# Kernel optimization log

Measured on AMD Instinct MI355X. Metric: run time of the kernel, lower is better.

Reference implementation:

```python
import jax, jax.numpy as jnp
import numpy as np

# BiDiGemma (Aveygo/SRNext) wrapping RecurrentGemma-style ResidualBlocks:
#   block0 = RECURRENT (causal conv width 4 + RG-LRU linear recurrence)
#   block1 = local (sliding-window, MQA) ATTENTION with partial RoPE
# Dropout(0.1) is treated as eval-mode identity.

B, S, D, H = 4, 4096, 256, 4
HD = D // H            # head dim = 64
E = 3 * D              # mlp_expanded_width = expand_ratio * dim
W_ATT = D              # attention_window_size = dim = 256 (divides S)
TW = 4                 # recurrentgemma temporal conv width
_NEG = -2.3819763e38   # recurrentgemma masking constant

_PNAMES = ["ln_gamma","ln_beta","proj_w","proj_b","fconv_w","fconv_b","bconv_w","bconv_b",
 "rn0_t","rn0_c","ly_w","ly_b","lx_w","lx_b","lo_w","lo_b","c1d_w","c1d_b",
 "a_param","ig_w","ig_b","ag_w","ag_b","mlp0_up_w","mlp0_up_b","mlp0_dn_w","mlp0_dn_b",
 "rn1_t","rn1_c","q_w","k_w","v_w","o_w","o_b","mlp1_up_w","mlp1_up_b","mlp1_dn_w","mlp1_dn_b"]


def _init_params(key):
    ks = iter(jax.random.split(key, 24))
    nrm = lambda shape, s: jax.random.normal(next(ks), shape, jnp.float32) * s
    p = {}
    p["ln_gamma"] = jnp.ones((D,), jnp.float32); p["ln_beta"] = jnp.zeros((D,), jnp.float32)
    p["proj_w"] = nrm((D, D), D ** -0.5);  p["proj_b"] = jnp.zeros((D,), jnp.float32)
    p["fconv_w"] = nrm((D, D), D ** -0.5); p["fconv_b"] = jnp.zeros((D,), jnp.float32)
    p["bconv_w"] = nrm((D, D), D ** -0.5); p["bconv_b"] = jnp.zeros((D,), jnp.float32)
    p["rn0_t"] = jnp.zeros((D,), jnp.float32); p["rn0_c"] = jnp.zeros((D,), jnp.float32)
    p["ly_w"] = nrm((D, D), D ** -0.5); p["ly_b"] = jnp.zeros((D,), jnp.float32)
    p["lx_w"] = nrm((D, D), D ** -0.5); p["lx_b"] = jnp.zeros((D,), jnp.float32)
    p["lo_w"] = nrm((D, D), D ** -0.5); p["lo_b"] = jnp.zeros((D,), jnp.float32)
    p["c1d_w"] = nrm((TW, D), 0.1);     p["c1d_b"] = jnp.zeros((D,), jnp.float32)
    p["a_param"] = jnp.log(jnp.expm1(jnp.linspace(0.9, 1.5, D, dtype=jnp.float32)))
    p["ig_w"] = nrm((H, HD, HD), HD ** -0.5); p["ig_b"] = jnp.zeros((H, HD), jnp.float32)
    p["ag_w"] = nrm((H, HD, HD), HD ** -0.5); p["ag_b"] = jnp.zeros((H, HD), jnp.float32)
    p["mlp0_up_w"] = nrm((2, D, E), D ** -0.5); p["mlp0_up_b"] = jnp.zeros((2, E), jnp.float32)
    p["mlp0_dn_w"] = nrm((E, D), E ** -0.5);    p["mlp0_dn_b"] = jnp.zeros((D,), jnp.float32)
    p["rn1_t"] = jnp.zeros((D,), jnp.float32); p["rn1_c"] = jnp.zeros((D,), jnp.float32)
    p["q_w"] = nrm((D, D), D ** -0.5); p["k_w"] = nrm((D, HD), D ** -0.5); p["v_w"] = nrm((D, HD), D ** -0.5)
    p["o_w"] = nrm((D, D), D ** -0.5); p["o_b"] = jnp.zeros((D,), jnp.float32)
    p["mlp1_up_w"] = nrm((2, D, E), D ** -0.5); p["mlp1_up_b"] = jnp.zeros((2, E), jnp.float32)
    p["mlp1_dn_w"] = nrm((E, D), E ** -0.5);    p["mlp1_dn_b"] = jnp.zeros((D,), jnp.float32)
    return p


def _gelu(x):
    return jax.nn.gelu(x, approximate=False)  # torch F.gelu default (erf)


def _rms_norm(x, scale, eps=1e-6):
    var = jnp.mean(jnp.square(x), axis=-1, keepdims=True)
    return x * jax.lax.rsqrt(var + eps) * (1.0 + scale)


def _layer_norm(x, g, b, eps=1e-5):
    m = jnp.mean(x, axis=-1, keepdims=True)
    v = jnp.mean(jnp.square(x - m), axis=-1, keepdims=True)
    return (x - m) * jax.lax.rsqrt(v + eps) * g + b


def _block_diag(x, w, b):
    # BlockDiagonalLinear: per-head [HD x HD] blocks
    xh = x.reshape(*x.shape[:-1], H, HD)
    y = jnp.einsum('bshd,hdk->bshk', xh, w) + b
    return y.reshape(*x.shape)


def _causal_conv1d(x, w, b):
    # depthwise causal conv, w: [TW, D], w[TW-1] multiplies current token
    xp = jnp.pad(x, ((0, 0), (TW - 1, 0), (0, 0)))
    out = sum(xp[:, i:i + x.shape[1], :] * w[i] for i in range(TW))
    return out + b


def _rg_lru(x, pos, a_param, ig_w, ig_b, ag_w, ag_b):
    gate_x = jax.nn.sigmoid(_block_diag(x, ig_w, ig_b))
    gate_a = jax.nn.sigmoid(_block_diag(x, ag_w, ag_b))
    log_a = -8.0 * gate_a * jax.nn.softplus(a_param)   # c = 8
    a = jnp.exp(log_a)
    mult = jnp.sqrt(-jnp.expm1(2.0 * log_a))           # sqrt(1 - a^2)
    reset = (pos == 0)[..., None]
    mult = jnp.where(reset, 1.0, mult)
    bterm = x * gate_x * mult
    def comb(e1, e2):
        a1, b1 = e1
        a2, b2 = e2
        return a1 * a2, a2 * b1 + b2
    _, h = jax.lax.associative_scan(comb, (a, bterm), axis=1)
    return h


def _rope(x, pos):
    # partial RoPE: applied to first half of head dim (recurrentgemma)
    rot, rest = jnp.split(x, 2, axis=-1)
    f = rot.shape[-1] // 2
    inv_freq = 10000.0 ** (-(2.0 / rot.shape[-1]) * jnp.arange(f, dtype=jnp.float32))
    t = pos[..., None, None].astype(jnp.float32) * inv_freq  # [b, s, 1, f]
    sin, cos = jnp.sin(t), jnp.cos(t)
    x1, x2 = jnp.split(rot, 2, axis=-1)
    return jnp.concatenate([x1 * cos - x2 * sin, x2 * cos + x1 * sin, rest], axis=-1)


def _local_attention(x, pos, q_w, k_w, v_w, o_w, o_b):
    # MQA sliding-window attention, window = W_ATT; chunked to honor locality
    b, s, _ = x.shape
    q = (x @ q_w).reshape(b, s, H, HD)
    k = (x @ k_w).reshape(b, s, 1, HD)
    v = (x @ v_w).reshape(b, s, HD)
    q = _rope(q, pos) * (HD ** -0.5)
    k = _rope(k, pos)[:, :, 0]
    Wn = W_ATT
    nb = s // Wn
    qc = q.reshape(b, nb, Wn, H, HD)
    kp = jnp.pad(k, ((0, 0), (Wn, 0), (0, 0))).reshape(b, nb + 1, Wn, HD)
    vp = jnp.pad(v, ((0, 0), (Wn, 0), (0, 0))).reshape(b, nb + 1, Wn, HD)
    kc = jnp.concatenate([kp[:, :-1], kp[:, 1:]], axis=2)  # [b, nb, 2W, HD]
    vc = jnp.concatenate([vp[:, :-1], vp[:, 1:]], axis=2)
    logits = jnp.einsum('bnqhd,bnkd->bnhqk', qc, kc)
    i = jnp.arange(Wn)[:, None]
    j = jnp.arange(2 * Wn)[None, :]
    diff = (i + Wn) - j                       # q_pos - k_pos
    base = (diff >= 0) & (diff <= Wn)         # causal & q <= k + window_size
    cidx = jnp.arange(nb)[:, None, None]
    mask = base[None] & ((cidx > 0) | (j[None] >= Wn))  # no left padding in chunk 0
    logits = jnp.where(mask[None, :, None], logits, _NEG)
    probs = jax.nn.softmax(logits, axis=-1)
    out = jnp.einsum('bnhqk,bnkd->bnqhd', probs, vc).reshape(b, s, D)
    return out @ o_w + o_b


def _mlp(x, up_w, up_b, dn_w, dn_b):
    up = jnp.einsum('bsd,cde->cbse', x, up_w) + up_b[:, None, None, :]
    act = _gelu(up[0]) * up[1]
    return act @ dn_w + dn_b


def _gemma_block(x, pos, p):
    # ResidualBlock 0: RECURRENT
    raw = x
    xn = _rms_norm(raw, p['rn0_t'])
    y = _gelu(xn @ p['ly_w'] + p['ly_b'])
    xr = xn @ p['lx_w'] + p['lx_b']
    xr = _causal_conv1d(xr, p['c1d_w'], p['c1d_b'])
    xr = _rg_lru(xr, pos, p['a_param'], p['ig_w'], p['ig_b'], p['ag_w'], p['ag_b'])
    xr = (xr * y) @ p['lo_w'] + p['lo_b']
    residual = xr + raw
    x = _rms_norm(residual, p['rn0_c'])
    x = _mlp(x, p['mlp0_up_w'], p['mlp0_up_b'], p['mlp0_dn_w'], p['mlp0_dn_b']) + residual
    # ResidualBlock 1: local ATTENTION
    raw = x
    xn = _rms_norm(raw, p['rn1_t'])
    xa = _local_attention(xn, pos, p['q_w'], p['k_w'], p['v_w'], p['o_w'], p['o_b'])
    residual = xa + raw
    x = _rms_norm(residual, p['rn1_c'])
    x = _mlp(x, p['mlp1_up_w'], p['mlp1_up_b'], p['mlp1_dn_w'], p['mlp1_dn_b']) + residual
    return x


def _forward(skip, *params):
    p = dict(zip(_PNAMES, params))
    b, s, _ = skip.shape
    pos = jnp.broadcast_to(jnp.arange(s, dtype=jnp.int32)[None], (b, s))
    x = _layer_norm(skip, p['ln_gamma'], p['ln_beta']) @ p['proj_w'] + p['proj_b']
    z = jax.nn.sigmoid(jnp.mean(jax.nn.silu(skip), axis=-1, keepdims=True))
    fwd = _gemma_block(x @ p['fconv_w'] + p['fconv_b'], pos, p)  # Conv1d k=1 == pointwise
    bwd = _gemma_block(x @ p['bconv_w'] + p['bconv_b'], pos, p)
    return z * (fwd + bwd) + skip


def setup_inputs() -> dict:
    key = jax.random.key(0)
    kx, kp = jax.random.split(key)
    inp = {"skip": jax.random.normal(kx, (B, S, D), jnp.float32)}
    inp.update(_init_params(kp))
    return inp


def reference(skip, ln_gamma, ln_beta, proj_w, proj_b, fconv_w, fconv_b, bconv_w, bconv_b, rn0_t, rn0_c, ly_w, ly_b, lx_w, lx_b, lo_w, lo_b, c1d_w, c1d_b, a_param, ig_w, ig_b, ag_w, ag_b, mlp0_up_w, mlp0_up_b, mlp0_dn_w, mlp0_dn_b, rn1_t, rn1_c, q_w, k_w, v_w, o_w, o_b, mlp1_up_w, mlp1_up_b, mlp1_dn_w, mlp1_dn_b):
    return _forward(skip, ln_gamma, ln_beta, proj_w, proj_b, fconv_w, fconv_b, bconv_w, bconv_b, rn0_t, rn0_c, ly_w, ly_b, lx_w, lx_b, lo_w, lo_b, c1d_w, c1d_b, a_param, ig_w, ig_b, ag_w, ag_b, mlp0_up_w, mlp0_up_b, mlp0_dn_w, mlp0_dn_b, rn1_t, rn1_c, q_w, k_w, v_w, o_w, o_b, mlp1_up_w, mlp1_up_b, mlp1_dn_w, mlp1_dn_b)
```

## Files before the change

kernel.cpp:

```cpp
#include <hip/hip_runtime.h>
#include <math.h>
#include <stddef.h>


#define BB   4
#define SS   4096
#define DD   256
#define HH   4
#define HDIM 64
#define EE   768
#define RR   (BB*SS)
#define RR2  (2*RR)
#define WNN  256
#define CH   64
#define NCH  (SS/CH)

typedef __attribute__((ext_vector_type(8))) short bfrag;
typedef __attribute__((ext_vector_type(4))) float f4acc;

__device__ __forceinline__ float geluf(float x){
  float u = 1.5957691216f*(x + 0.044715f*x*x*x);
  float e = __expf(u);
  float t = 1.f - 2.f/(e+1.f);
  return 0.5f*x*(1.f+t);
// ... 179 lines not shown
      if constexpr(TERMS>=2){
        *(float4*)&Bsl[d0] = *(const float4*)(pB0l0 + k0);
        *(float4*)&Bsl[d1] = *(const float4*)(pB0l1 + k0);
      }
    } else {
      *(float4*)&Bsh[d0] = *(const float4*)(pBa + k0);
      if constexpr(TERMS>=2) *(float4*)&Bsl[d0] = *(const float4*)(pBb + k0);
      if constexpr(DUAL){
        *(float4*)&B2h[d0] = *(const float4*)(pBc + k0);
        if constexpr(TERMS>=2) *(float4*)&B2l[d0] = *(const float4*)(pBd + k0);
      }
    }
    __syncthreads();

    bfrag ah[4], al[TERMS==3?4:1], b0hf[NT], b0lf[TERMS>=2?NT:1];
    bfrag b1hf[DUAL?NT:1], b1lf[(DUAL&&TERMS>=2)?NT:1];
#pragma unroll
    for(int mi=0;mi<4;mi++){
      int row = wm*64 + mi*16 + m16;
      ah[mi] = *(const bfrag*)&Ash[row*ST + q*8];
      if constexpr(TERMS==3) al[mi] = *(const bfrag*)&Asl[row*ST + q*8];
    }
#pragma unroll
    for(int ni=0;ni<NT;ni++){
      int n = wn*(BN/2) + ni*16 + m16;
      b0hf[ni] = *(const bfrag*)&Bsh[n*ST + q*8];
      if constexpr(TERMS>=2) b0lf[ni] = *(const bfrag*)&Bsl[n*ST + q*8];
      if constexpr(DUAL){
        b1hf[ni] = *(const bfrag*)&B2h[n*ST + q*8];
        if constexpr(TERMS>=2) b1lf[ni] = *(const bfrag*)&B2l[n*ST + q*8];
      }
    }
#pragma unroll
    for(int mi=0;mi<4;mi++)
#pragma unroll
      for(int ni=0;ni<NT;ni++){
        acc[mi][ni] = __builtin_amdgcn_mfma_f32_16x16x32_bf16(ah[mi], b0hf[ni], acc[mi][ni],0,0,0);
        if constexpr(TERMS>=2)
          acc[mi][ni] = __builtin_amdgcn_mfma_f32_16x16x32_bf16(ah[mi], b0lf[ni], acc[mi][ni],0,0,0);
        if constexpr(TERMS==3)
          acc[mi][ni] = __builtin_amdgcn_mfma_f32_16x16x32_bf16(al[mi], b0hf[ni], acc[mi][ni],0,0,0);
        if constexpr(DUAL){
          acc2[mi][ni] = __builtin_amdgcn_mfma_f32_16x16x32_bf16(ah[mi], b1hf[ni], acc2[mi][ni],0,0,0);
          if constexpr(TERMS>=2)
            acc2[mi][ni] = __builtin_amdgcn_mfma_f32_16x16x32_bf16(ah[mi], b1lf[ni], acc2[mi][ni],0,0,0);
          if constexpr(TERMS==3)
            acc2[mi][ni] = __builtin_amdgcn_mfma_f32_16x16x32_bf16(al[mi], b1hf[ni], acc2[mi][ni],0,0,0);
        }
      }
    __syncthreads();
  }

  if constexpr(OUT==0 || OUT==1 || OUT==5){
#pragma unroll
    for(int ni=0;ni<NT;ni++){
      const int col = bn + wn*(BN/2) + ni*16 + m16;
      float bv0 = (MODE&1) ? bias0[col] : 0.f;
      float bv1 = DUAL ? bias1[col] : 0.f;
#pragma unroll
      for(int mi=0;mi<4;mi++){
#pragma unroll
        for(int r=0;r<4;r++){
          const int row = bm + wm*64 + mi*16 + q*4 + r;
          float v = acc[mi][ni][r] + bv0;
          if constexpr(DUAL){
            float v2 = acc2[mi][ni][r] + bv1;
            v = geluf(v) * v2;
          } else if(MODE&2){
            v = geluf(v);
          }
          if(MODE&8) v += Res[(size_t)row*ldc + col];
          if constexpr(OUT==0){
            C[(size_t)row*ldc + col] = v;
          } else if constexpr(OUT==1){
            unsigned short hb = f2bf(v);
            Ch[(size_t)row*ldc + col] = hb;
            Cl[(size_t)row*ldc + col] = f2bf(v - bf2f(hb));
          } else {
            Ch[(size_t)row*ldc + col] = f2bf(v);
          }
        }
      }
    }
  } else if constexpr(OUT==2){
    const int hb = bn + wn*64;
    const float p = (float)m16;
    const float invf = __expf(-p * 0.575646273248511f);
#pragma unroll
    for(int mi=0;mi<4;mi++){
#pragma unroll
      for(int r=0;r<4;r++){
        const int row = bm + wm*64 + mi*16 + q*4 + r;
        const int s = row & (SS-1);
        float t = (float)s * invf;
        float sn, cs; __sincosf(t, &sn, &cs);
        float x1 = acc[mi][0][r], x2 = acc[mi][1][r];
        float v0 = (x1*cs - x2*sn)*0.125f;
        float v1 = (x2*cs + x1*sn)*0.125f;
        float v2 = acc[mi][2][r]*0.125f;
        float v3 = acc[mi][3][r]*0.125f;
        size_t base = (size_t)row*ldc + hb;
        unsigned short hh;
        hh=f2bf(v0); Ch[base+m16]=hh;    Cl[base+m16]   =f2bf(v0-bf2f(hh));
        hh=f2bf(v1); Ch[base+16+m16]=hh; Cl[base+16+m16]=f2bf(v1-bf2f(hh));
        hh=f2bf(v2); Ch[base+32+m16]=hh; Cl[base+32+m16]=f2bf(v2-bf2f(hh));
        hh=f2bf(v3); Ch[base+48+m16]=hh; Cl[base+48+m16]=f2bf(v3-bf2f(hh));
      }
    }
  } else if constexpr(OUT==3){
    const float p = (float)m16;
    const float invf = __expf(-p * 0.575646273248511f);
#pragma unroll
    for(int mi=0;mi<4;mi++){
#pragma unroll
      for(int r=0;r<4;r++){
        const int row = bm + wm*64 + mi*16 + q*4 + r;
        const int s = row & (SS-1);
        float v0, v1;
        if(wn==0){
          float t = (float)s * invf;
          float sn, cs; __sincosf(t, &sn, &cs);
          float x1 = acc[mi][0][r], x2 = acc[mi][1][r];
          v0 = x1*cs - x2*sn;
          v1 = x2*cs + x1*sn;
        } else {
          v0 = acc[mi][0][r]; v1 = acc[mi][1][r];
        }
        size_t base = (size_t)row*ldc + wn*32;
        unsigned short hh;
        hh=f2bf(v0); Ch[base+m16]=hh;    Cl[base+m16]   =f2bf(v0-bf2f(hh));
        hh=f2bf(v1); Ch[base+16+m16]=hh; Cl[base+16+m16]=f2bf(v1-bf2f(hh));
      }
    }
  } else if constexpr(OUT==4){
#pragma unroll
    for(int ni=0;ni<NT;ni++){
      const int col = wn*32 + ni*16 + m16;
#pragma unroll
      for(int mi=0;mi<4;mi++){
        const int rowb = bm + wm*64 + mi*16 + q*4;
        const int b = rowb >> 12, sl = rowb & (SS-1);
        ushort4 hv;
        hv.x = f2bf(acc[mi][ni][0]); hv.y = f2bf(acc[mi][ni][1]);
        hv.z = f2bf(acc[mi][ni][2]); hv.w = f2bf(acc[mi][ni][3]);
        *(ushort4*)(Ch + ((size_t)(b*64 + col))*SS + sl) = hv;
      }
    }
  } else if constexpr(OUT==7){
    const float p = (float)m16;
    const float invf = __expf(-p * 0.575646273248511f);
#pragma unroll
    for(int mi=0;mi<4;mi++){
#pragma unroll
      for(int r=0;r<4;r++){
        const int row = bm + wm*64 + mi*16 + q*4 + r;
        const int s = row & (SS-1);
        float v0, v1;
        if(wn==0){
          float t = (float)s * invf;
          float sn, cs; __sincosf(t, &sn, &cs);
          float x1 = acc[mi][0][r], x2 = acc[mi][1][r];
          v0 = x1*cs - x2*sn;
          v1 = x2*cs + x1*sn;
        } else {
          v0 = acc[mi][0][r]; v1 = acc[mi][1][r];
        }
        size_t base = (size_t)row*ldc + wn*32;
        unsigned short hh;
        hh=f2bf(v0); Ch[base+m16]=hh;    Cl[base+m16]   =f2bf(v0-bf2f(hh));
        hh=f2bf(v1); Ch[base+16+m16]=hh; Cl[base+16+m16]=f2bf(v1-bf2f(hh));
      }
    }
    if constexpr(DUAL){
      unsigned short* Cv = (unsigned short*)C;
#pragma unroll
      for(int ni=0;ni<NT;ni++){
        const int col = wn*32 + ni*16 + m16;
#pragma unroll
        for(int mi=0;mi<4;mi++){
          const int rowb = bm + wm*64 + mi*16 + q*4;
          const int b = rowb >> 12, sl = rowb & (SS-1);
          ushort4 hv;
          hv.x = f2bf(acc2[mi][ni][0]); hv.y = f2bf(acc2[mi][ni][1]);
          hv.z = f2bf(acc2[mi][ni][2]); hv.w = f2bf(acc2[mi][ni][3]);
          *(ushort4*)(Cv + ((size_t)(b*64 + col))*SS + sl) = hv;
        }
      }
    }
  }
}

__global__ __launch_bounds__(256) void gates_conv_k(
    const float* __restrict__ X,
    const float* __restrict__ cw, const float* __restrict__ cb,
    const unsigned short* __restrict__ igth, const unsigned short* __restrict__ igtl,
    const unsigned short* __restrict__ agth, const unsigned short* __restrict__ agtl,
    const float* __restrict__ igb, const float* __restrict__ agb,
    const float* __restrict__ ap,
    float* __restrict__ Aout, float* __restrict__ Bout)
{
  constexpr int ST = 72;
  __shared__ unsigned short Ash[128*ST];
  __shared__ unsigned short Asl[128*ST];

  const int h  = blockIdx.x;
  const int bm = blockIdx.y*128;
  const int tid = threadIdx.x;
  const int lane = tid & 63, wave = tid >> 6;
  const int wm = wave >> 1, wn = wave & 1;
  const int m16 = lane & 15, q = lane >> 4;

  {
    const int strip = tid >> 4;
    const int cg = (tid & 15)*4;
    const int col0 = h*HDIM + cg;
    const int r0 = bm + strip*8;
    float h0[4], h1[4], h2[4];
#pragma unroll
    for(int i=0;i<3;i++){
      int rr = r0 - 3 + i;
      int rc = rr < 0 ? 0 : rr;
      float4 hv = *(const float4*)(X + (size_t)rc*DD + col0);
      float* dst = (i==0)?h0:((i==1)?h1:h2);
      dst[0]=hv.x; dst[1]=hv.y; dst[2]=hv.z; dst[3]=hv.w;
    }
    float4 w0v = *(const float4*)(cw + 0*DD + col0);
    float4 w1v = *(const float4*)(cw + 1*DD + col0);
    float4 w2v = *(const float4*)(cw + 2*DD + col0);
    float4 w3v = *(const float4*)(cw + 3*DD + col0);
    float4 bbv = *(const float4*)(cb + col0);
    const float* w0 = (const float*)&w0v; const float* w1 = (const float*)&w1v;
    const float* w2 = (const float*)&w2v; const float* w3 = (const float*)&w3v;
    const float* bb = (const float*)&bbv;
    for(int rr=0; rr<8; rr++){
      const int r = r0 + rr;
      const int s = r & (SS-1);
      float4 cv = *(const float4*)(X + (size_t)r*DD + col0);
      float cur[4]; cur[0]=cv.x; cur[1]=cv.y; cur[2]=cv.z; cur[3]=cv.w;
      ushort4 hi, lo;
      unsigned short* hp = (unsigned short*)&hi;
      unsigned short* lp = (unsigned short*)&lo;
#pragma unroll
      for(int j=0;j<4;j++){
        float acc = bb[j] + w3[j]*cur[j];
        if(s>=1) acc += w2[j]*h2[j];
        if(s>=2) acc += w1[j]*h1[j];
        if(s>=3) acc += w0[j]*h0[j];
        unsigned short hb = f2bf(acc);
        hp[j] = hb; lp[j] = f2bf(acc - bf2f(hb));
      }
      const int dst = (strip*8+rr)*ST + cg;
      *(ushort4*)&Ash[dst] = hi;
      *(ushort4*)&Asl[dst] = lo;
#pragma unroll
      for(int j=0;j<4;j++){ h0[j]=h1[j]; h1[j]=h2[j]; h2[j]=cur[j]; }
    }
  }
  __syncthreads();

  f4acc accI[4][2], accA[4][2];
#pragma unroll
  for(int i=0;i<4;i++)
#pragma unroll
    for(int j=0;j<2;j++){ accI[i][j]=(f4acc)0.f; accA[i][j]=(f4acc)0.f; }

  const size_t wbase = (size_t)h*HDIM*HDIM;
#pragma unroll
  for(int ks=0;ks<2;ks++){
    bfrag ah[4], al[4];
#pragma unroll
    for(int mi=0;mi<4;mi++){
      const int row = wm*64 + mi*16 + m16;
      ah[mi] = *(const bfrag*)&Ash[row*ST + ks*32 + q*8];
      al[mi] = *(const bfrag*)&Asl[row*ST + ks*32 + q*8];
    }
#pragma unroll
    for(int ni=0;ni<2;ni++){
      const size_t bo = wbase + (size_t)(wn*32 + ni*16 + m16)*HDIM + ks*32 + q*8;
      bfrag bIh = *(const bfrag*)(igth + bo);
      bfrag bIl = *(const bfrag*)(igtl + bo);
      bfrag bAh = *(const bfrag*)(agth + bo);
      bfrag bAl = *(const bfrag*)(agtl + bo);
#pragma unroll
      for(int mi=0;mi<4;mi++){
        accI[mi][ni] = __builtin_amdgcn_mfma_f32_16x16x32_bf16(ah[mi], bIh, accI[mi][ni],0,0,0);
        accI[mi][ni] = __builtin_amdgcn_mfma_f32_16x16x32_bf16(ah[mi], bIl, accI[mi][ni],0,0,0);
        accI[mi][ni] = __builtin_amdgcn_mfma_f32_16x16x32_bf16(al[mi], bIh, accI[mi][ni],0,0,0);
        accA[mi][ni] = __builtin_amdgcn_mfma_f32_16x16x32_bf16(ah[mi], bAh, accA[mi][ni],0,0,0);
        accA[mi][ni] = __builtin_amdgcn_mfma_f32_16x16x32_bf16(ah[mi], bAl, accA[mi][ni],0,0,0);
        accA[mi][ni] = __builtin_amdgcn_mfma_f32_16x16x32_bf16(al[mi], bAh, accA[mi][ni],0,0,0);
      }
    }
  }

#pragma unroll
  for(int ni=0;ni<2;ni++){
    const int cl  = wn*32 + ni*16 + m16;
    const int col = h*HDIM + cl;
    const float bI = igb[col], bA = agb[col];
    const float apv = ap[col];
    const float sp = (apv > 20.f) ? apv : log1pf(expf(apv));
#pragma unroll
    for(int mi=0;mi<4;mi++){
#pragma unroll
      for(int r=0;r<4;r++){
        const int lrow = wm*64 + mi*16 + q*4 + r;
        const int row = bm + lrow;
        const int s = row & (SS-1);
        float gx = 1.f/(1.f + __expf(-(accI[mi][ni][r] + bI)));
        float ga = 1.f/(1.f + __expf(-(accA[mi][ni][r] + bA)));
        float la = -8.f * ga * sp;
        float a_ = __expf(la);
        float mult = (s==0) ? 1.f : sqrtf(fmaxf(1.f - __expf(2.f*la), 0.f));
        float x = bf2f(Ash[lrow*ST + cl]) + bf2f(Asl[lrow*ST + cl]);
        Aout[(size_t)row*DD + col] = a_;
        Bout[(size_t)row*DD + col] = x * gx * mult;
      }
    }
  }
}

__global__ __launch_bounds__(256) void scan1_k(const float* __restrict__ A,
    const float* __restrict__ Bv, float* __restrict__ csa, float* __restrict__ csb)
{
  int idx = blockIdx.x*256 + threadIdx.x;
  int d = idx & (DD-1);
  int c = (idx >> 8) & (NCH-1);
  int b = idx >> 14;
  size_t base = ((size_t)b*SS + (size_t)c*CH)*DD + d;
  float Aa = 1.f, Bb_ = 0.f;
  for(int t=0;t<CH;t++){
    float a  = A [base + (size_t)t*DD];
    float bb = Bv[base + (size_t)t*DD];
    Aa  = a*Aa;
    Bb_ = a*Bb_ + bb;
  }
  csa[idx] = Aa; csb[idx] = Bb_;
}

__global__ __launch_bounds__(256) void scan2_k(const float* __restrict__ csa,
    float* __restrict__ csb)
{
  int idx = blockIdx.x*256 + threadIdx.x;
  int d = idx & (DD-1);
  int b = idx >> 8;
  float h = 0.f;
  for(int c=0;c<NCH;c++){
    size_t i = ((size_t)b*NCH + c)*DD + d;
    float Aa = csa[i], Bb_ = csb[i];
    csb[i] = h;
    h = Aa*h + Bb_;
  }
}

__global__ __launch_bounds__(256) void scan3_k(const float* __restrict__ A,
    const float* __restrict__ Bv, const float* __restrict__ csb,
    const unsigned short* __restrict__ Yh,
    unsigned short* __restrict__ Hh)
{
  int idx = blockIdx.x*256 + threadIdx.x;
  int d = idx & (DD-1);
  int c = (idx >> 8) & (NCH-1);
  int b = idx >> 14;
  size_t base = ((size_t)b*SS + (size_t)c*CH)*DD + d;
  float h = csb[idx];
  for(int t=0;t<CH;t++){
    float a  = A [base + (size_t)t*DD];
    float bb = Bv[base + (size_t)t*DD];
    h = a*h + bb;
    float v = h * bf2f(Yh[base + (size_t)t*DD]);
    Hh[base + (size_t)t*DD] = f2bf(v);
  }
}

#define AST 72
__global__ __launch_bounds__(256) void attn_k(
    const unsigned short* __restrict__ Qh, const unsigned short* __restrict__ Ql,
    const unsigned short* __restrict__ Kh, const unsigned short* __restrict__ Kl,
    const unsigned short* __restrict__ Vt,
    unsigned short* __restrict__ Oh, unsigned short* __restrict__ Ol)
{
  __shared__ unsigned short Ksh[64*AST], Ksl[64*AST], Vsh[64*AST];
  __shared__ unsigned short Ps[4*16*AST];

  const int qt = blockIdx.x & 3, n = blockIdx.x >> 2;
  const int h = blockIdx.y, b = blockIdx.z;
  const int tid = threadIdx.x;
  const int lane = tid & 63, w = tid >> 6;
  const int m16 = lane & 15, q = lane >> 4;
  const int s0 = n*WNN + qt*64;

  const size_t qro = ((size_t)(b*SS + s0 + w*16 + m16))*DD + h*HDIM + q*8;
  bfrag qh0 = *(const bfrag*)(Qh + qro);
  bfrag qh1 = *(const bfrag*)(Qh + qro + 32);
  bfrag ql0 = *(const bfrag*)(Ql + qro);
  bfrag ql1 = *(const bfrag*)(Ql + qro + 32);

  float mrow[4], lrow[4];
  f4acc oacc[4];
#pragma unroll
  for(int i=0;i<4;i++){ mrow[i]=-3.0e38f; lrow[i]=0.f; oacc[i]=(f4acc)0.f; }

  const int ktlo = (n==0) ? 4 : qt;
  const int kthi = qt + 4;
  const int sr = tid >> 2, sc = tid & 3;

  for(int kt=ktlo; kt<=kthi; kt++){
    const int kbase = (n-1)*WNN + kt*64;
#pragma unroll
    for(int cc=0; cc<2; cc++){
      int g = sc + cc*4;
      *(float4*)&Ksh[sr*AST + g*8] =
        *(const float4*)(Kh + (size_t)(b*SS + kbase + sr)*HDIM + g*8);
      *(float4*)&Ksl[sr*AST + g*8] =
        *(const float4*)(Kl + (size_t)(b*SS + kbase + sr)*HDIM + g*8);
      *(float4*)&Vsh[sr*AST + g*8] =
        *(const float4*)(Vt + ((size_t)(b*64 + sr))*SS + kbase + g*8);
    }
    __syncthreads();

    f4acc sacc[4];
#pragma unroll
    for(int nt=0;nt<4;nt++) sacc[nt] = (f4acc)0.f;
#pragma unroll
    for(int nt=0;nt<4;nt++){
      const int kr = (nt*16+m16)*AST;
      bfrag kh0 = *(const bfrag*)&Ksh[kr + q*8];
      bfrag kh1 = *(const bfrag*)&Ksh[kr + 32 + q*8];
      bfrag kl0 = *(const bfrag*)&Ksl[kr + q*8];
      bfrag kl1 = *(const bfrag*)&Ksl[kr + 32 + q*8];
      sacc[nt] = __builtin_amdgcn_mfma_f32_16x16x32_bf16(qh0, kh0, sacc[nt],0,0,0);
      sacc[nt] = __builtin_amdgcn_mfma_f32_16x16x32_bf16(qh0, kl0, sacc[nt],0,0,0);
      sacc[nt] = __builtin_amdgcn_mfma_f32_16x16x32_bf16(ql0, kh0, sacc[nt],0,0,0);
      sacc[nt] = __builtin_amdgcn_mfma_f32_16x16x32_bf16(qh1, kh1, sacc[nt],0,0,0);
      sacc[nt] = __builtin_amdgcn_mfma_f32_16x16x32_bf16(qh1, kl1, sacc[nt],0,0,0);
      sacc[nt] = __builtin_amdgcn_mfma_f32_16x16x32_bf16(ql1, kh1, sacc[nt],0,0,0);
    }

    const bool needlo = (kt == qt+4);
    const bool needhi = (kt == qt);
#pragma unroll
    for(int r=0;r<4;r++){
      int qp = qt*64 + w*16 + q*4 + r;
      float sv[4];
      float tm = -3.0e38f;
#pragma unroll
      for(int nt=0;nt<4;nt++){
        float scv = sacc[nt][r];
        if(needlo || needhi){
          int kj = kt*64 + nt*16 + m16;
          int diff = qp + WNN - kj;
          bool ok = (!needlo || diff >= 0) && (!needhi || diff <= WNN);
          scv = ok ? scv : -3.0e38f;
        }
        sv[nt] = scv;
        tm = fmaxf(tm, scv);
      }
#pragma unroll
      for(int off=1; off<16; off<<=1) tm = fmaxf(tm, __shfl_xor(tm, off, 64));
      float mn = fmaxf(mrow[r], tm);
      float alpha = __expf(mrow[r]-mn);
      float rs = 0.f;
#pragma unroll
      for(int nt=0;nt<4;nt++){
        float pp = __expf(sv[nt]-mn);
        rs += pp;
        Ps[w*16*AST + (q*4+r)*AST + nt*16 + m16] = f2bf(pp);
      }
#pragma unroll
      for(int off=1; off<16; off<<=1) rs += __shfl_xor(rs, off, 64);
      lrow[r] = lrow[r]*alpha + rs;
      mrow[r] = mn;
#pragma unroll
      for(int nt=0;nt<4;nt++) oacc[nt][r] *= alpha;
    }

#pragma unroll
    for(int s=0;s<2;s++){
      bfrag pa = *(const bfrag*)&Ps[w*16*AST + m16*AST + s*32 + q*8];
#pragma unroll
      for(int nt=0;nt<4;nt++){
        bfrag vh_ = *(const bfrag*)&Vsh[(nt*16+m16)*AST + s*32 + q*8];
        oacc[nt] = __builtin_amdgcn_mfma_f32_16x16x32_bf16(pa, vh_, oacc[nt],0,0,0);
      }
    }
    __syncthreads();
  }

#pragma unroll
  for(int r=0;r<4;r++){
    float invl = 1.f/lrow[r];
    const size_t rowbase = ((size_t)(b*SS + s0 + w*16 + q*4 + r))*DD + h*HDIM;
#pragma unroll
    for(int nt=0;nt<4;nt++){
      float v = oacc[nt][r]*invl;
      unsigned short hb = f2bf(v);
      Oh[rowbase + nt*16 + m16] = hb;
      Ol[rowbase + nt*16 + m16] = f2bf(v - bf2f(hb));
    }
  }
}

__global__ __launch_bounds__(256) void comb_k(const float* __restrict__ of,
    const float* __restrict__ ob, const float* __restrict__ z,
    const float* __restrict__ skip, float* __restrict__ out)
{
  int idx = blockIdx.x*256 + threadIdx.x;
  int r = idx >> 8;
  out[idx] = z[r]*(of[idx]+ob[idx]) + skip[idx];
}

struct Params {
  const float *ln_gamma,*ln_beta,*proj_w,*proj_b,*fconv_w,*fconv_b,*bconv_w,*bconv_b,
    *rn0_t,*rn0_c,*ly_w,*ly_b,*lx_w,*lx_b,*lo_w,*lo_b,*c1d_w,*c1d_b,*a_param,
    *ig_w,*ig_b,*ag_w,*ag_b,*mlp0_up_w,*mlp0_up_b,*mlp0_dn_w,*mlp0_dn_b,
    *rn1_t,*rn1_c,*q_w,*k_w,*v_w,*o_w,*o_b,*mlp1_up_w,*mlp1_up_b,*mlp1_dn_w,*mlp1_dn_b;
};

struct WSplit {
  unsigned short *proj_h,*proj_l,*fconv_h,*fconv_l,*bconv_h,*bconv_l,
    *ly_h,*ly_l,*lx_h,*lx_l,*lo_h,*lo_l,*q_h,*q_l,*o_h,*o_l,
    *k_h,*k_l,*v_h,*v_l,
    *up0a_h,*up0a_l,*up0b_h,*up0b_l,*up1a_h,*up1a_l,*up1b_h,*up1b_l,
    *dn0_h,*dn0_l,*dn1_h,*dn1_l,
    *igt_h,*igt_l,*agt_h,*agt_l;
};

#define USN ((unsigned short*)nullptr)

extern "C" void kernel_launch(void* const* d_in, const int* in_sizes, int n_in,
                              void* d_out, int out_size, void* d_ws, size_t ws_size,
                              hipStream_t stream)
{
  (void)in_sizes; (void)n_in; (void)out_size; (void)ws_size;
  const float* skip = (const float*)d_in[0];
  Params p;
  p.ln_gamma  =(const float*)d_in[1];  p.ln_beta  =(const float*)d_in[2];
  p.proj_w    =(const float*)d_in[3];  p.proj_b   =(const float*)d_in[4];
  p.fconv_w   =(const float*)d_in[5];  p.fconv_b  =(const float*)d_in[6];
  p.bconv_w   =(const float*)d_in[7];  p.bconv_b  =(const float*)d_in[8];
  p.rn0_t     =(const float*)d_in[9];  p.rn0_c    =(const float*)d_in[10];
  p.ly_w      =(const float*)d_in[11]; p.ly_b     =(const float*)d_in[12];
  p.lx_w      =(const float*)d_in[13]; p.lx_b     =(const float*)d_in[14];
  p.lo_w      =(const float*)d_in[15]; p.lo_b     =(const float*)d_in[16];
  p.c1d_w     =(const float*)d_in[17]; p.c1d_b    =(const float*)d_in[18];
  p.a_param   =(const float*)d_in[19];
  p.ig_w      =(const float*)d_in[20]; p.ig_b     =(const float*)d_in[21];
  p.ag_w      =(const float*)d_in[22]; p.ag_b     =(const float*)d_in[23];
  p.mlp0_up_w =(const float*)d_in[24]; p.mlp0_up_b=(const float*)d_in[25];
  p.mlp0_dn_w =(const float*)d_in[26]; p.mlp0_dn_b=(const float*)d_in[27];
  p.rn1_t     =(const float*)d_in[28]; p.rn1_c    =(const float*)d_in[29];
  p.q_w       =(const float*)d_in[30]; p.k_w      =(const float*)d_in[31];
  p.v_w       =(const float*)d_in[32]; p.o_w      =(const float*)d_in[33];
  p.o_b       =(const float*)d_in[34];
  p.mlp1_up_w =(const float*)d_in[35]; p.mlp1_up_b=(const float*)d_in[36];
  p.mlp1_dn_w =(const float*)d_in[37]; p.mlp1_dn_b=(const float*)d_in[38];

  float* ws = (float*)d_ws;
  const size_t RD  = (size_t)RR*DD;
  const size_t PD2 = (size_t)RR2*DD;
  size_t off = 0;
  float* Z   = ws + off; off += 16384;
  float* XB2 = ws + off; off += 2*RD;
  float* CV2 = ws + off; off += 2*RD;
  float* W1  = ws + off; off += 2*RD;
  float* W2  = ws + off; off += 2*RD;
  float* W3  = ws + off; off += RD;
  float* W4  = ws + off; off += 2*RD;

  float* CSA = CV2;
  float* CSB = CV2 + 8*NCH*DD;

  unsigned short* NPh = (unsigned short*)W4;  unsigned short* NPl = NPh + PD2;
  float* BT = W4;
  unsigned short* HYh = (unsigned short*)W1;
  unsigned short* X0h = (unsigned short*)W1;  unsigned short* X0l = X0h + (size_t)RR*DD;
  float* XR2 = W1;
  unsigned short* Qph = (unsigned short*)W1;  unsigned short* Qpl = Qph + PD2;
  float* Abuf = W2;
  unsigned short* P2h = (unsigned short*)W2;  unsigned short* P2l = P2h + PD2;
  unsigned short* Yh  = (unsigned short*)W3;
  unsigned short* KPh = (unsigned short*)W3;  unsigned short* KPl = KPh + (size_t)RR2*HDIM;
  unsigned short* Vt  = KPl + (size_t)RR2*HDIM;
  unsigned short* ACTh = (unsigned short*)W1;
  float* OUT2 = XB2;

  unsigned short* sp = (unsigned short*)(ws + off);
  WSplit w;
  auto alloc_s = [&](size_t n){ unsigned short* r = sp; sp += n; return r; };
  const size_t SDD = (size_t)DD*DD, SKV = (size_t)DD*HDIM, SUP = (size_t)DD*EE;
  const size_t SBD = (size_t)HH*HDIM*HDIM;
  w.proj_h=alloc_s(SDD);  w.proj_l=alloc_s(SDD);
  w.fconv_h=alloc_s(SDD); w.fconv_l=alloc_s(SDD);
  w.bconv_h=alloc_s(SDD); w.bconv_l=alloc_s(SDD);
  w.ly_h=alloc_s(SDD);    w.ly_l=alloc_s(SDD);
  w.lx_h=alloc_s(SDD);    w.lx_l=alloc_s(SDD);
  w.lo_h=alloc_s(SDD);    w.lo_l=alloc_s(SDD);
  w.q_h=alloc_s(SDD);     w.q_l=alloc_s(SDD);
  w.o_h=alloc_s(SDD);     w.o_l=alloc_s(SDD);
  w.k_h=alloc_s(SKV);     w.k_l=alloc_s(SKV);
  w.v_h=alloc_s(SKV);     w.v_l=alloc_s(SKV);
  w.up0a_h=alloc_s(SUP);  w.up0a_l=alloc_s(SUP);
  w.up0b_h=alloc_s(SUP);  w.up0b_l=alloc_s(SUP);
  w.up1a_h=alloc_s(SUP);  w.up1a_l=alloc_s(SUP);
  w.up1b_h=alloc_s(SUP);  w.up1b_l=alloc_s(SUP);
  w.dn0_h=alloc_s(SUP);   w.dn0_l=alloc_s(SUP);
  w.dn1_h=alloc_s(SUP);   w.dn1_l=alloc_s(SUP);
  w.igt_h=alloc_s(SBD);   w.igt_l=alloc_s(SBD);
  w.agt_h=alloc_s(SBD);   w.agt_l=alloc_s(SBD);

  dim3 blk(256);
  dim3 g2(2,128,1);
  dim3 g2m(2,256,1), g64m(1,256,1), gdual(12,256,1);
  dim3 ggm(HH, RR2/128, 1);

  {
    TS8 ga;
    ga.t[0] = {p.proj_w,  w.proj_h,  w.proj_l,  DD, DD};
    ga.t[1] = {p.fconv_w, w.fconv_h, w.fconv_l, DD, DD};
    ga.t[2] = {p.bconv_w, w.bconv_h, w.bconv_l, DD, DD};
    ga.t[3] = {p.ly_w,    w.ly_h,    w.ly_l,    DD, DD};
    ga.t[4] = {p.lx_w,    w.lx_h,    w.lx_l,    DD, DD};
    ga.t[5] = {p.lo_w,    w.lo_h,    w.lo_l,    DD, DD};
    ga.t[6] = {p.q_w,     w.q_h,     w.q_l,     DD, DD};
    ga.t[7] = {p.o_w,     w.o_h,     w.o_l,     DD, DD};
    tsplit8_k<<<dim3(DD*DD/256, 8), blk, 0, stream>>>(ga);
    TS8 gb;
    gb.t[0] = {p.k_w,              w.k_h,    w.k_l,    DD, HDIM};
    gb.t[1] = {p.v_w,              w.v_h,    w.v_l,    DD, HDIM};
    gb.t[2] = {p.mlp0_up_w,        w.up0a_h, w.up0a_l, DD, EE};
    gb.t[3] = {p.mlp0_up_w+(size_t)DD*EE, w.up0b_h, w.up0b_l, DD, EE};
    gb.t[4] = {p.mlp1_up_w,        w.up1a_h, w.up1a_l, DD, EE};
    gb.t[5] = {p.mlp1_up_w+(size_t)DD*EE, w.up1b_h, w.up1b_l, DD, EE};
    gb.t[6] = {p.mlp0_dn_w,        w.dn0_h,  w.dn0_l,  EE, DD};
    gb.t[7] = {p.mlp1_dn_w,        w.dn1_h,  w.dn1_l,  EE, DD};
    tsplit8_k<<<dim3(DD*EE/256, 8), blk, 0, stream>>>(gb);
    TS8 gc;
    for(int h=0;h<HH;h++){
      gc.t[h]   = {p.ig_w + (size_t)h*HDIM*HDIM, w.igt_h + (size_t)h*HDIM*HDIM,
                   w.igt_l + (size_t)h*HDIM*HDIM, HDIM, HDIM};
      gc.t[4+h] = {p.ag_w + (size_t)h*HDIM*HDIM, w.agt_h + (size_t)h*HDIM*HDIM,
                   w.agt_l + (size_t)h*HDIM*HDIM, HDIM, HDIM};
    }
    tsplit8_k<<<dim3(HDIM*HDIM/256, 8), blk, 0, stream>>>(gc);
  }

  ln_z_k<<<RR/4, blk, 0, stream>>>(skip, p.ln_gamma, p.ln_beta, NPh, NPl, Z);
  gemm_mfma<128,1,0,1,3><<<g2,blk,0,stream>>>(NPh,NPl, w.proj_h,w.proj_l, USN,USN,
      p.proj_b,nullptr,nullptr, nullptr, X0h, X0l, DD,DD,DD);
  gemm_mfma<128,1,0,0,3><<<g2,blk,0,stream>>>(X0h,X0l, w.fconv_h,w.fconv_l, USN,USN,
      p.fconv_b,nullptr,nullptr, XB2, USN,USN, DD,DD,DD);
  gemm_mfma<128,1,0,0,3><<<g2,blk,0,stream>>>(X0h,X0l, w.bconv_h,w.bconv_l, USN,USN,
      p.bconv_b,nullptr,nullptr, XB2 + RD, USN,USN, DD,DD,DD);

  rms_h_k<<<RR2/4, blk, 0, stream>>>(XB2, p.rn0_t, NPh);
  gemm_mfma<128,3,0,5,2><<<g2m,blk,0,stream>>>(NPh,USN, w.ly_h,w.ly_l, USN,USN,
      p.ly_b,nullptr,nullptr, nullptr, Yh, USN, DD,DD,DD);
  gemm_mfma<128,1,0,0,2><<<g2m,blk,0,stream>>>(NPh,USN, w.lx_h,w.lx_l, USN,USN,
      p.lx_b,nullptr,nullptr, XR2, USN,USN, DD,DD,DD);
  gates_conv_k<<<ggm,blk,0,stream>>>(XR2, p.c1d_w, p.c1d_b,
      w.igt_h, w.igt_l, w.agt_h, w.agt_l, p.ig_b, p.ag_b, p.a_param, Abuf, BT);
  scan1_k<<<8*NCH*DD/256, blk,0,stream>>>(Abuf, BT, CSA, CSB);
  scan2_k<<<8*DD/256, blk,0,stream>>>(CSA, CSB);
  scan3_k<<<8*NCH*DD/256, blk,0,stream>>>(Abuf, BT, CSB, Yh, HYh);
  gemm_mfma<128,9,0,0,2><<<g2m,blk,0,stream>>>(HYh,USN, w.lo_h,w.lo_l, USN,USN,
      p.lo_b,nullptr, XB2, CV2, USN,USN, DD,DD,DD);
  rms_h_k<<<RR2/4,blk,0,stream>>>(CV2, p.rn0_c, NPh);
  gemm_mfma<64,1,1,5,1><<<gdual,blk,0,stream>>>(NPh,USN, w.up0a_h,USN,
      w.up0b_h,USN, p.mlp0_up_b, p.mlp0_up_b+EE, nullptr, nullptr,
      ACTh, USN, DD,DD,EE);
  gemm_mfma<128,9,0,0,2><<<g2m,blk,0,stream>>>(ACTh,USN, w.dn0_h,w.dn0_l, USN,USN,
      p.mlp0_dn_b,nullptr, CV2, XB2, USN,USN, EE,EE,DD);

  rms_k<<<RR2/4,blk,0,stream>>>(XB2, p.rn1_t, NPh, NPl);
  gemm_mfma<128,0,0,2,2><<<g2m,blk,0,stream>>>(NPh,USN, w.q_h,w.q_l, USN,USN,
      nullptr,nullptr,nullptr, nullptr, Qph, Qpl, DD,DD,DD);
  gemm_mfma<64,0,1,7,3><<<g64m,blk,0,stream>>>(NPh,NPl, w.k_h,w.k_l, w.v_h,w.v_l,
      nullptr,nullptr,nullptr, (float*)Vt, KPh, KPl, DD,DD,HDIM);
  attn_k<<<dim3(64,4,8),blk,0,stream>>>(Qph, Qpl, KPh, KPl, Vt, P2h, P2l);
  gemm_mfma<128,9,0,0,2><<<g2m,blk,0,stream>>>(P2h,USN, w.o_h,w.o_l, USN,USN,
      p.o_b,nullptr, XB2, CV2, USN,USN, DD,DD,DD);
  rms_h_k<<<RR2/4,blk,0,stream>>>(CV2, p.rn1_c, NPh);
  gemm_mfma<64,1,1,5,1><<<gdual,blk,0,stream>>>(NPh,USN, w.up1a_h,USN,
      w.up1b_h,USN, p.mlp1_up_b, p.mlp1_up_b+EE, nullptr, nullptr,
      ACTh, USN, DD,DD,EE);
  gemm_mfma<128,9,0,0,2><<<g2m,blk,0,stream>>>(ACTh,USN, w.dn1_h,w.dn1_l, USN,USN,
      p.mlp1_dn_b,nullptr, CV2, XB2, USN,USN, EE,EE,DD);

  comb_k<<<RR*DD/256, blk, 0, stream>>>(OUT2, OUT2 + RD, Z, skip, (float*)d_out);
}
```

Measured before the change: 711.7 us.

## Process two query tiles per attention block and stage gated MLP output through LDS

The attention kernel now handles two adjacent 64-row query tiles per block, so each loaded K/V tile is reused by both and the grid is halved. This cuts redundant K/V global loads and barrier counts, at the cost of more registers and a per-tile reload of the second tile's Q fragments. The dual up-projection GEMM gets a new epilogue (OUT==6) that writes GELU-gated bf16 results into shared memory and then stores them with 16-byte row-contiguous writes instead of scattered 2-byte stores.

```diff
diff --git a/kernel.cpp b/kernel.cpp
--- a/kernel.cpp
+++ b/kernel.cpp
@@ -285,6 +285,37 @@
         }
       }
     }
+  } else if constexpr(OUT==6){
+    unsigned short* Tsh = Ash;
+#pragma unroll
+    for(int half=0; half<2; half++){
+      if(wm == half){
+#pragma unroll
+        for(int ni=0;ni<NT;ni++){
+          const int lcol = wn*(BN/2) + ni*16 + m16;
+          const int col = bn + lcol;
+          const float bv0 = bias0[col], bv1 = bias1[col];
+#pragma unroll
+          for(int mi=0;mi<4;mi++){
+#pragma unroll
+            for(int r=0;r<4;r++){
+              const int lr = mi*16 + q*4 + r;
+              float v = geluf(acc[mi][ni][r]+bv0) * (acc2[mi][ni][r]+bv1);
+              Tsh[lr*72 + lcol] = f2bf(v);
+            }
+          }
+        }
+      }
+      __syncthreads();
+      {
+        const int row = tid>>2, cc0 = (tid&3)*16;
+        unsigned short* dst = Ch + (size_t)(bm + half*64 + row)*ldc + bn + cc0;
+        const unsigned short* src = &Tsh[row*72 + cc0];
+        *(float4*)(dst)     = *(const float4*)(src);
+        *(float4*)(dst + 8) = *(const float4*)(src + 8);
+      }
+      __syncthreads();
+    }
   } else if constexpr(OUT==2){
     const int hb = bn + wn*64;
     const float p = (float)m16;
@@ -577,6 +608,73 @@
 }
 
 #define AST 72
+
+#define ATTN_PROC(QH0,QH1,QL0,QL1,QTV,MR,LR,OA) do{                            \
+    f4acc sacc[4];                                                             \
+    _Pragma("unroll")                                                          \
+    for(int nt=0;nt<4;nt++) sacc[nt] = (f4acc)0.f;                             \
+    _Pragma("unroll")                                                          \
+    for(int nt=0;nt<4;nt++){                                                   \
+      const int kr = (nt*16+m16)*AST;                                          \
+      bfrag kh0 = *(const bfrag*)&Ksh[kr + q*8];                               \
+      bfrag kh1 = *(const bfrag*)&Ksh[kr + 32 + q*8];                          \
+      bfrag kl0 = *(const bfrag*)&Ksl[kr + q*8];                               \
+      bfrag kl1 = *(const bfrag*)&Ksl[kr + 32 + q*8];                          \
+      sacc[nt] = __builtin_amdgcn_mfma_f32_16x16x32_bf16((QH0), kh0, sacc[nt],0,0,0); \
+      sacc[nt] = __builtin_amdgcn_mfma_f32_16x16x32_bf16((QH0), kl0, sacc[nt],0,0,0); \
+      sacc[nt] = __builtin_amdgcn_mfma_f32_16x16x32_bf16((QL0), kh0, sacc[nt],0,0,0); \
+      sacc[nt] = __builtin_amdgcn_mfma_f32_16x16x32_bf16((QH1), kh1, sacc[nt],0,0,0); \
+      sacc[nt] = __builtin_amdgcn_mfma_f32_16x16x32_bf16((QH1), kl1, sacc[nt],0,0,0); \
+      sacc[nt] = __builtin_amdgcn_mfma_f32_16x16x32_bf16((QL1), kh1, sacc[nt],0,0,0); \
+    }                                                                          \
+    const bool needlo = (kt == (QTV)+4);                                       \
+    const bool needhi = (kt == (QTV));                                         \
+    _Pragma("unroll")                                                          \
+    for(int r=0;r<4;r++){                                                      \
+      int qp = (QTV)*64 + w*16 + q*4 + r;                                      \
+      float sv[4];                                                             \
+      float tm = -3.0e38f;                                                     \
+      _Pragma("unroll")                                                        \
+      for(int nt=0;nt<4;nt++){                                                 \
+        float scv = sacc[nt][r];                                               \
+        if(needlo || needhi){                                                  \
+          int kj = kt*64 + nt*16 + m16;                                        \
+          int diff = qp + WNN - kj;                                            \
+          bool ok = (!needlo || diff >= 0) && (!needhi || diff <= WNN);        \
+          scv = ok ? scv : -3.0e38f;                                           \
+        }                                                                      \
+        sv[nt] = scv;                                                          \
+        tm = fmaxf(tm, scv);                                                   \
+      }                                                                        \
+      _Pragma("unroll")                                                        \
+      for(int off=1; off<16; off<<=1) tm = fmaxf(tm, __shfl_xor(tm, off, 64)); \
+      float mn = fmaxf((MR)[r], tm);                                           \
+      float alpha = __expf((MR)[r]-mn);                                        \
+      float rs = 0.f;                                                          \
+      _Pragma("unroll")                                                        \
+      for(int nt=0;nt<4;nt++){                                                 \
+        float pp = __expf(sv[nt]-mn);                                          \
+        rs += pp;                                                              \
+        Ps[w*16*AST + (q*4+r)*AST + nt*16 + m16] = f2bf(pp);                   \
+      }                                                                        \
+      _Pragma("unroll")                                                        \
+      for(int off=1; off<16; off<<=1) rs += __shfl_xor(rs, off, 64);           \
+      (LR)[r] = (LR)[r]*alpha + rs;                                            \
+      (MR)[r] = mn;                                                            \
+      _Pragma("unroll")                                                        \
+      for(int nt=0;nt<4;nt++) (OA)[nt][r] *= alpha;                            \
+    }                                                                          \
+    _Pragma("unroll")                                                          \
+    for(int s=0;s<2;s++){                                                      \
+      bfrag pa = *(const bfrag*)&Ps[w*16*AST + m16*AST + s*32 + q*8];          \
+      _Pragma("unroll")                                                        \
+      for(int nt=0;nt<4;nt++){                                                 \
+        bfrag vh_ = *(const bfrag*)&Vsh[(nt*16+m16)*AST + s*32 + q*8];         \
+        (OA)[nt] = __builtin_amdgcn_mfma_f32_16x16x32_bf16(pa, vh_, (OA)[nt],0,0,0); \
+      }                                                                        \
+    }                                                                          \
+  }while(0)
+
 __global__ __launch_bounds__(256) void attn_k(
     const unsigned short* __restrict__ Qh, const unsigned short* __restrict__ Ql,
     const unsigned short* __restrict__ Kh, const unsigned short* __restrict__ Kl,
@@ -586,26 +684,31 @@
   __shared__ unsigned short Ksh[64*AST], Ksl[64*AST], Vsh[64*AST];
   __shared__ unsigned short Ps[4*16*AST];
 
-  const int qt = blockIdx.x & 3, n = blockIdx.x >> 2;
+  const int qt2 = blockIdx.x & 1, n = blockIdx.x >> 1;
   const int h = blockIdx.y, b = blockIdx.z;
   const int tid = threadIdx.x;
   const int lane = tid & 63, w = tid >> 6;
   const int m16 = lane & 15, q = lane >> 4;
-  const int s0 = n*WNN + qt*64;
-
-  const size_t qro = ((size_t)(b*SS + s0 + w*16 + m16))*DD + h*HDIM + q*8;
-  bfrag qh0 = *(const bfrag*)(Qh + qro);
-  bfrag qh1 = *(const bfrag*)(Qh + qro + 32);
-  bfrag ql0 = *(const bfrag*)(Ql + qro);
-  bfrag ql1 = *(const bfrag*)(Ql + qro + 32);
-
-  float mrow[4], lrow[4];
-  f4acc oacc[4];
-#pragma unroll
-  for(int i=0;i<4;i++){ mrow[i]=-3.0e38f; lrow[i]=0.f; oacc[i]=(f4acc)0.f; }
-
-  const int ktlo = (n==0) ? 4 : qt;
-  const int kthi = qt + 4;
+  const int qa = qt2*2, qb = qa+1;
+  const int s0a = n*WNN + qa*64;
+
+  const size_t qroA = ((size_t)(b*SS + s0a + w*16 + m16))*DD + h*HDIM + q*8;
+  const size_t qroB = qroA + (size_t)64*DD;
+  bfrag qh0a = *(const bfrag*)(Qh + qroA);
+  bfrag qh1a = *(const bfrag*)(Qh + qroA + 32);
+  bfrag ql0a = *(const bfrag*)(Ql + qroA);
+  bfrag ql1a = *(const bfrag*)(Ql + qroA + 32);
+
+  float mrA[4], lrA[4], mrB[4], lrB[4];
+  f4acc oaA[4], oaB[4];
+#pragma unroll
+  for(int i=0;i<4;i++){
+    mrA[i]=-3.0e38f; lrA[i]=0.f; oaA[i]=(f4acc)0.f;
+    mrB[i]=-3.0e38f; lrB[i]=0.f; oaB[i]=(f4acc)0.f;
+  }
+
+  const int ktlo = (n==0) ? 4 : qa;
+  const int kthi = qb + 4;
   const int sr = tid >> 2, sc = tid & 3;
 
   for(int kt=ktlo; kt<=kthi; kt++){
@@ -622,84 +725,35 @@
     }
     __syncthreads();
 
-    f4acc sacc[4];
-#pragma unroll
-    for(int nt=0;nt<4;nt++) sacc[nt] = (f4acc)0.f;
+    if(kt <= qa+4){
+      ATTN_PROC(qh0a, qh1a, ql0a, ql1a, qa, mrA, lrA, oaA);
+    }
+    if(kt >= qb){
+      bfrag qh0b = *(const bfrag*)(Qh + qroB);
+      bfrag qh1b = *(const bfrag*)(Qh + qroB + 32);
+      bfrag ql0b = *(const bfrag*)(Ql + qroB);
+      bfrag ql1b = *(const bfrag*)(Ql + qroB + 32);
+      ATTN_PROC(qh0b, qh1b, ql0b, ql1b, qb, mrB, lrB, oaB);
+    }
+    __syncthreads();
+  }
+
+#pragma unroll
+  for(int r=0;r<4;r++){
+    float invlA = 1.f/lrA[r];
+    float invlB = 1.f/lrB[r];
+    const size_t rbA = ((size_t)(b*SS + s0a + w*16 + q*4 + r))*DD + h*HDIM;
+    const size_t rbB = rbA + (size_t)64*DD;
 #pragma unroll
     for(int nt=0;nt<4;nt++){
-      const int kr = (nt*16+m16)*AST;
-      bfrag kh0 = *(const bfrag*)&Ksh[kr + q*8];
-      bfrag kh1 = *(const bfrag*)&Ksh[kr + 32 + q*8];
-      bfrag kl0 = *(const bfrag*)&Ksl[kr + q*8];
-      bfrag kl1 = *(const bfrag*)&Ksl[kr + 32 + q*8];
-      sacc[nt] = __builtin_amdgcn_mfma_f32_16x16x32_bf16(qh0, kh0, sacc[nt],0,0,0);
-      sacc[nt] = __builtin_amdgcn_mfma_f32_16x16x32_bf16(qh0, kl0, sacc[nt],0,0,0);
-      sacc[nt] = __builtin_amdgcn_mfma_f32_16x16x32_bf16(ql0, kh0, sacc[nt],0,0,0);
-      sacc[nt] = __builtin_amdgcn_mfma_f32_16x16x32_bf16(qh1, kh1, sacc[nt],0,0,0);
-      sacc[nt] = __builtin_amdgcn_mfma_f32_16x16x32_bf16(qh1, kl1, sacc[nt],0,0,0);
-      sacc[nt] = __builtin_amdgcn_mfma_f32_16x16x32_bf16(ql1, kh1, sacc[nt],0,0,0);
-    }
-
-    const bool needlo = (kt == qt+4);
-    const bool needhi = (kt == qt);
-#pragma unroll
-    for(int r=0;r<4;r++){
-      int qp = qt*64 + w*16 + q*4 + r;
-      float sv[4];
-      float tm = -3.0e38f;
-#pragma unroll
-      for(int nt=0;nt<4;nt++){
-        float scv = sacc[nt][r];
-        if(needlo || needhi){
-          int kj = kt*64 + nt*16 + m16;
-          int diff = qp + WNN - kj;
-          bool ok = (!needlo || diff >= 0) && (!needhi || diff <= WNN);
-          scv = ok ? scv : -3.0e38f;
-        }
-        sv[nt] = scv;
-        tm = fmaxf(tm, scv);
-      }
-#pragma unroll
-      for(int off=1; off<16; off<<=1) tm = fmaxf(tm, __shfl_xor(tm, off, 64));
-      float mn = fmaxf(mrow[r], tm);
-      float alpha = __expf(mrow[r]-mn);
-      float rs = 0.f;
-#pragma unroll
-      for(int nt=0;nt<4;nt++){
-        float pp = __expf(sv[nt]-mn);
-        rs += pp;
-        Ps[w*16*AST + (q*4+r)*AST + nt*16 + m16] = f2bf(pp);
-      }
-#pragma unroll
-      for(int off=1; off<16; off<<=1) rs += __shfl_xor(rs, off, 64);
-      lrow[r] = lrow[r]*alpha + rs;
-      mrow[r] = mn;
-#pragma unroll
-      for(int nt=0;nt<4;nt++) oacc[nt][r] *= alpha;
-    }
-
-#pragma unroll
-    for(int s=0;s<2;s++){
-      bfrag pa = *(const bfrag*)&Ps[w*16*AST + m16*AST + s*32 + q*8];
-#pragma unroll
-      for(int nt=0;nt<4;nt++){
-        bfrag vh_ = *(const bfrag*)&Vsh[(nt*16+m16)*AST + s*32 + q*8];
-        oacc[nt] = __builtin_amdgcn_mfma_f32_16x16x32_bf16(pa, vh_, oacc[nt],0,0,0);
-      }
-    }
-    __syncthreads();
-  }
-
-#pragma unroll
-  for(int r=0;r<4;r++){
-    float invl = 1.f/lrow[r];
-    const size_t rowbase = ((size_t)(b*SS + s0 + w*16 + q*4 + r))*DD + h*HDIM;
-#pragma unroll
-    for(int nt=0;nt<4;nt++){
-      float v = oacc[nt][r]*invl;
-      unsigned short hb = f2bf(v);
-      Oh[rowbase + nt*16 + m16] = hb;
-      Ol[rowbase + nt*16 + m16] = f2bf(v - bf2f(hb));
+      float vA = oaA[nt][r]*invlA;
+      unsigned short hA = f2bf(vA);
+      Oh[rbA + nt*16 + m16] = hA;
+      Ol[rbA + nt*16 + m16] = f2bf(vA - bf2f(hA));
+      float vB = oaB[nt][r]*invlB;
+      unsigned short hB = f2bf(vB);
+      Oh[rbB + nt*16 + m16] = hB;
+      Ol[rbB + nt*16 + m16] = f2bf(vB - bf2f(hB));
     }
   }
 }
@@ -869,7 +923,7 @@
   gemm_mfma<128,9,0,0,2><<<g2m,blk,0,stream>>>(HYh,USN, w.lo_h,w.lo_l, USN,USN,
       p.lo_b,nullptr, XB2, CV2, USN,USN, DD,DD,DD);
   rms_h_k<<<RR2/4,blk,0,stream>>>(CV2, p.rn0_c, NPh);
-  gemm_mfma<64,1,1,5,1><<<gdual,blk,0,stream>>>(NPh,USN, w.up0a_h,USN,
+  gemm_mfma<64,1,1,6,1><<<gdual,blk,0,stream>>>(NPh,USN, w.up0a_h,USN,
       w.up0b_h,USN, p.mlp0_up_b, p.mlp0_up_b+EE, nullptr, nullptr,
       ACTh, USN, DD,DD,EE);
   gemm_mfma<128,9,0,0,2><<<g2m,blk,0,stream>>>(ACTh,USN, w.dn0_h,w.dn0_l, USN,USN,
@@ -880,11 +934,11 @@
       nullptr,nullptr,nullptr, nullptr, Qph, Qpl, DD,DD,DD);
   gemm_mfma<64,0,1,7,3><<<g64m,blk,0,stream>>>(NPh,NPl, w.k_h,w.k_l, w.v_h,w.v_l,
       nullptr,nullptr,nullptr, (float*)Vt, KPh, KPl, DD,DD,HDIM);
-  attn_k<<<dim3(64,4,8),blk,0,stream>>>(Qph, Qpl, KPh, KPl, Vt, P2h, P2l);
+  attn_k<<<dim3(32,4,8),blk,0,stream>>>(Qph, Qpl, KPh, KPl, Vt, P2h, P2l);
   gemm_mfma<128,9,0,0,2><<<g2m,blk,0,stream>>>(P2h,USN, w.o_h,w.o_l, USN,USN,
       p.o_b,nullptr, XB2, CV2, USN,USN, DD,DD,DD);
   rms_h_k<<<RR2/4,blk,0,stream>>>(CV2, p.rn1_c, NPh);
-  gemm_mfma<64,1,1,5,1><<<gdual,blk,0,stream>>>(NPh,USN, w.up1a_h,USN,
+  gemm_mfma<64,1,1,6,1><<<gdual,blk,0,stream>>>(NPh,USN, w.up1a_h,USN,
       w.up1b_h,USN, p.mlp1_up_b, p.mlp1_up_b+EE, nullptr, nullptr,
       ACTh, USN, DD,DD,EE);
   gemm_mfma<128,9,0,0,2><<<g2m,blk,0,stream>>>(ACTh,USN, w.dn1_h,w.dn1_l, USN,USN,
```

Measured after the change: 926.8 us. 1.3x slower.

## Fuse chunk-level scan reduction into gates_conv epilogue, drop scan1 kernel

Applied to the files above, without the earlier changes.

The gates kernel now computes per-64-row chunk products and affine composites of the RG-LRU recurrence in registers, combining lane segments with cross-lane shuffles. It writes csa/csb directly, so the separate scan1 pass, which re-read the full A and B buffers, is removed. This saves one kernel launch and a full read of two large fp32 buffers. The cost is extra shuffles and serial multiply work in the epilogue. Correctness depends on each wave's 64 rows matching the CH=64 chunk boundaries.

```diff
diff --git a/kernel.cpp b/kernel.cpp
--- a/kernel.cpp
+++ b/kernel.cpp
@@ -400,7 +400,8 @@
     const unsigned short* __restrict__ agth, const unsigned short* __restrict__ agtl,
     const float* __restrict__ igb, const float* __restrict__ agb,
     const float* __restrict__ ap,
-    float* __restrict__ Aout, float* __restrict__ Bout)
+    float* __restrict__ Aout, float* __restrict__ Bout,
+    float* __restrict__ csa, float* __restrict__ csb)
 {
   constexpr int ST = 72;
   __shared__ unsigned short Ash[128*ST];
@@ -503,8 +504,10 @@
     const float bI = igb[col], bA = agb[col];
     const float apv = ap[col];
     const float sp = (apv > 20.f) ? apv : log1pf(expf(apv));
+    float segA[4], segB[4];
 #pragma unroll
     for(int mi=0;mi<4;mi++){
+      float sA = 1.f, sB = 0.f;
 #pragma unroll
       for(int r=0;r<4;r++){
         const int lrow = wm*64 + mi*16 + q*4 + r;
@@ -516,29 +519,31 @@
         float a_ = __expf(la);
         float mult = (s==0) ? 1.f : sqrtf(fmaxf(1.f - __expf(2.f*la), 0.f));
         float x = bf2f(Ash[lrow*ST + cl]) + bf2f(Asl[lrow*ST + cl]);
+        float bt = x * gx * mult;
         Aout[(size_t)row*DD + col] = a_;
-        Bout[(size_t)row*DD + col] = x * gx * mult;
-      }
-    }
-  }
-}
-
-__global__ __launch_bounds__(256) void scan1_k(const float* __restrict__ A,
-    const float* __restrict__ Bv, float* __restrict__ csa, float* __restrict__ csb)
-{
-  int idx = blockIdx.x*256 + threadIdx.x;
-  int d = idx & (DD-1);
-  int c = (idx >> 8) & (NCH-1);
-  int b = idx >> 14;
-  size_t base = ((size_t)b*SS + (size_t)c*CH)*DD + d;
-  float Aa = 1.f, Bb_ = 0.f;
-  for(int t=0;t<CH;t++){
-    float a  = A [base + (size_t)t*DD];
-    float bb = Bv[base + (size_t)t*DD];
-    Aa  = a*Aa;
-    Bb_ = a*Bb_ + bb;
-  }
-  csa[idx] = Aa; csb[idx] = Bb_;
+        Bout[(size_t)row*DD + col] = bt;
+        sA = a_ * sA;
+        sB = a_ * sB + bt;
+      }
+      segA[mi] = sA; segB[mi] = sB;
+    }
+    float TA = 1.f, TB = 0.f;
+#pragma unroll
+    for(int mi=0;mi<4;mi++){
+#pragma unroll
+      for(int qq=0;qq<4;qq++){
+        float A = __shfl(segA[mi], qq*16 + m16, 64);
+        float B = __shfl(segB[mi], qq*16 + m16, 64);
+        TA = A * TA;
+        TB = A * TB + B;
+      }
+    }
+    if(q == 0){
+      const size_t cidx = (size_t)((bm + wm*64) >> 6)*DD + col;
+      csa[cidx] = TA;
+      csb[cidx] = TB;
+    }
+  }
 }
 
 __global__ __launch_bounds__(256) void scan2_k(const float* __restrict__ csa,
@@ -862,8 +867,8 @@
   gemm_mfma<128,1,0,0,2><<<g2m,blk,0,stream>>>(NPh,USN, w.lx_h,w.lx_l, USN,USN,
       p.lx_b,nullptr,nullptr, XR2, USN,USN, DD,DD,DD);
   gates_conv_k<<<ggm,blk,0,stream>>>(XR2, p.c1d_w, p.c1d_b,
-      w.igt_h, w.igt_l, w.agt_h, w.agt_l, p.ig_b, p.ag_b, p.a_param, Abuf, BT);
-  scan1_k<<<8*NCH*DD/256, blk,0,stream>>>(Abuf, BT, CSA, CSB);
+      w.igt_h, w.igt_l, w.agt_h, w.agt_l, p.ig_b, p.ag_b, p.a_param,
+      Abuf, BT, CSA, CSB);
   scan2_k<<<8*DD/256, blk,0,stream>>>(CSA, CSB);
   scan3_k<<<8*NCH*DD/256, blk,0,stream>>>(Abuf, BT, CSB, Yh, HYh);
   gemm_mfma<128,9,0,0,2><<<g2m,blk,0,stream>>>(HYh,USN, w.lo_h,w.lo_l, USN,USN,
```

Result: slower. 843.4 us (+18.5%).
